# Kernel tuning notes

Measured on AMD Instinct MI355X. Metric: run time of the kernel, lower is better.

## Reference

```python
import jax, jax.numpy as jnp
import numpy as np

CUTOFF = 5.0
MAX_NUM_PAIRS = 131072
N_ATOMS = 4096
BOX_L = 40.0


def setup_inputs() -> dict:
    key = jax.random.key(0)
    k1, _ = jax.random.split(key)
    positions = jax.random.uniform(k1, (N_ATOMS, 3), dtype=jnp.float32) * BOX_L
    box = jnp.eye(3, dtype=jnp.float32) * BOX_L  # triclinic box vectors (rows)
    return {"positions": positions, "box": box}


def _min_image_deltas(positions, box):
    # delta[i, j] = positions[i] - positions[j], wrapped by the minimum image
    # convention: subtract the nearest integer multiple of the box vectors.
    delta = positions[:, None, :] - positions[None, :, :]  # [N, N, 3]
    inv_box = jnp.linalg.inv(box)
    frac = delta @ inv_box                                  # fractional coords
    delta = delta - jnp.round(frac) @ box
    return delta


def reference(positions, box):
    n = positions.shape[0]
    delta = _min_image_deltas(positions, box)               # [N, N, 3]
    dist2 = jnp.sum(delta * delta, axis=-1)                 # [N, N]

    idx = jnp.arange(n)
    upper = idx[:, None] < idx[None, :]                     # unique pairs i<j
    mask = upper & (dist2 < CUTOFF * CUTOFF)

    n_pairs = jnp.sum(mask).astype(jnp.int32)
    # Compact hit pairs into a fixed-size buffer (static shape for jit).
    flat_idx, = jnp.nonzero(mask.ravel(), size=MAX_NUM_PAIRS, fill_value=0)
    valid = jnp.arange(MAX_NUM_PAIRS) < n_pairs

    pair_i = jnp.where(valid, flat_idx // n, -1)
    pair_j = jnp.where(valid, flat_idx % n, -1)
    pairs = jnp.stack([pair_i, pair_j], axis=0)             # [2, P]

    deltas = jnp.where(valid[:, None], delta.reshape(n * n, 3)[flat_idx], 0.0)
    d2 = jnp.where(valid, dist2.ravel()[flat_idx], 1.0)     # safe sqrt on pads
    distances = jnp.where(valid, jnp.sqrt(d2), 0.0)

    return pairs, deltas, distances, n_pairs
```

## Files before the change

### kernel.cpp

```cpp
#include <hip/hip_runtime.h>


#define CUT2 25.0f

__device__ __forceinline__ void load_box_inv(const float* __restrict__ box,
                                             float B[3][3], float Binv[3][3]) {
    #pragma unroll
    for (int r = 0; r < 3; ++r)
        #pragma unroll
        for (int c = 0; c < 3; ++c)
            B[r][c] = box[r * 3 + c];

    float a00 = B[0][0], a01 = B[0][1], a02 = B[0][2];
    float a10 = B[1][0], a11 = B[1][1], a12 = B[1][2];
    float a20 = B[2][0], a21 = B[2][1], a22 = B[2][2];

    float adj00 =  (a11 * a22 - a12 * a21);
    float adj01 = -(a01 * a22 - a02 * a21);
    float adj02 =  (a01 * a12 - a02 * a11);
    float adj10 = -(a10 * a22 - a12 * a20);
    float adj11 =  (a00 * a22 - a02 * a20);
    float adj12 = -(a00 * a12 - a02 * a10);
    float adj20 =  (a10 * a21 - a11 * a20);
    float adj21 = -(a00 * a21 - a01 * a20);
    float adj22 =  (a00 * a11 - a01 * a10);

    float det = a00 * adj00 + a01 * adj10 + a02 * adj20;

    Binv[0][0] = __fdiv_rn(adj00, det); Binv[0][1] = __fdiv_rn(adj01, det); Binv[0][2] = __fdiv_rn(adj02, det);
    Binv[1][0] = __fdiv_rn(adj10, det); Binv[1][1] = __fdiv_rn(adj11, det); Binv[1][2] = __fdiv_rn(adj12, det);
    Binv[2][0] = __fdiv_rn(adj20, det); Binv[2][1] = __fdiv_rn(adj21, det); Binv[2][2] = __fdiv_rn(adj22, det);
}

__device__ __forceinline__ void min_image(float xi, float yi, float zi,
                                          float xj, float yj, float zj,
                                          const float B[3][3], const float Binv[3][3],
                                          float& dx, float& dy, float& dz, float& d2) {
    dx = __fsub_rn(xi, xj);
    dy = __fsub_rn(yi, yj);
    dz = __fsub_rn(zi, zj);

    float f0 = __fadd_rn(__fadd_rn(__fmul_rn(dx, Binv[0][0]), __fmul_rn(dy, Binv[1][0])), __fmul_rn(dz, Binv[2][0]));
    float f1 = __fadd_rn(__fadd_rn(__fmul_rn(dx, Binv[0][1]), __fmul_rn(dy, Binv[1][1])), __fmul_rn(dz, Binv[2][1]));
    float f2 = __fadd_rn(__fadd_rn(__fmul_rn(dx, Binv[0][2]), __fmul_rn(dy, Binv[1][2])), __fmul_rn(dz, Binv[2][2]));

    float r0 = rintf(f0), r1 = rintf(f1), r2 = rintf(f2);

    float c0 = __fadd_rn(__fadd_rn(__fmul_rn(r0, B[0][0]), __fmul_rn(r1, B[1][0])), __fmul_rn(r2, B[2][0]));
    float c1 = __fadd_rn(__fadd_rn(__fmul_rn(r0, B[0][1]), __fmul_rn(r1, B[1][1])), __fmul_rn(r2, B[2][1]));
    float c2 = __fadd_rn(__fadd_rn(__fmul_rn(r0, B[0][2]), __fmul_rn(r1, B[1][2])), __fmul_rn(r2, B[2][2]));

    dx = __fsub_rn(dx, c0);
    dy = __fsub_rn(dy, c1);
    dz = __fsub_rn(dz, c2);

    d2 = __fadd_rn(__fadd_rn(__fmul_rn(dx, dx), __fmul_rn(dy, dy)), __fmul_rn(dz, dz));
}

__device__ __forceinline__ int count_row_lds(int i, int lane,
                                             const float* __restrict__ spos,
                                             const float B[3][3], const float Binv[3][3],
                                             unsigned long long* __restrict__ mrow,
                                             int nchunks) {
    float xi = spos[3 * i + 0], yi = spos[3 * i + 1], zi = spos[3 * i + 2];
    int c0 = i >> 6;
    int cnt = 0;

    {
        int j = (c0 << 6) + lane;
        bool hit = false;
        if (j > i) {
            float dx, dy, dz, d2;
            min_image(xi, yi, zi, spos[3 * j + 0], spos[3 * j + 1], spos[3 * j + 2],
                      B, Binv, dx, dy, dz, d2);
            hit = (d2 < CUT2);
        }
        unsigned long long m = __ballot(hit);
        if (lane == 0) mrow[c0] = m;
        cnt += __popcll(m);
    }

    int c = c0 + 1;
    for (; c + 4 <= nchunks; c += 4) {
        int j0 = (c << 6) + lane;
        float dx0, dy0, dz0, d20, dx1, dy1, dz1, d21;
        float dx2, dy2, dz2, d22, dx3, dy3, dz3, d23;
        min_image(xi, yi, zi, spos[3 * j0 + 0],   spos[3 * j0 + 1],   spos[3 * j0 + 2],   B, Binv, dx0, dy0, dz0, d20);
        min_image(xi, yi, zi, spos[3 * j0 + 192], spos[3 * j0 + 193], spos[3 * j0 + 194], B, Binv, dx1, dy1, dz1, d21);
        min_image(xi, yi, zi, spos[3 * j0 + 384], spos[3 * j0 + 385], spos[3 * j0 + 386], B, Binv, dx2, dy2, dz2, d22);
        min_image(xi, yi, zi, spos[3 * j0 + 576], spos[3 * j0 + 577], spos[3 * j0 + 578], B, Binv, dx3, dy3, dz3, d23);
        unsigned long long m0 = __ballot(d20 < CUT2);
        unsigned long long m1 = __ballot(d21 < CUT2);
        unsigned long long m2 = __ballot(d22 < CUT2);
        unsigned long long m3 = __ballot(d23 < CUT2);
        if (lane == 0) { mrow[c] = m0; mrow[c + 1] = m1; mrow[c + 2] = m2; mrow[c + 3] = m3; }
        cnt += __popcll(m0) + __popcll(m1) + __popcll(m2) + __popcll(m3);
    }
    for (; c < nchunks; ++c) {
        int j = (c << 6) + lane;
        float dx, dy, dz, d2;
        min_image(xi, yi, zi, spos[3 * j + 0], spos[3 * j + 1], spos[3 * j + 2],
                  B, Binv, dx, dy, dz, d2);
        unsigned long long m = __ballot(d2 < CUT2);
        if (lane == 0) mrow[c] = m;
        cnt += __popcll(m);
    }
    return cnt;
}

__global__ void __launch_bounds__(256)
k1_pad_count(const float* __restrict__ pos, const float* __restrict__ box,
             float* __restrict__ out, int* __restrict__ counts,
             unsigned long long* __restrict__ masks, int N, int P) {
    __shared__ float spos[12288];

    int tid = blockIdx.x * blockDim.x + threadIdx.x;
    int nthreads = gridDim.x * blockDim.x;

    int total = 6 * P + 1;
    for (int k = tid; k < total; k += nthreads)
        out[k] = (k < 2 * P) ? -1.0f : 0.0f;

    for (int k = threadIdx.x; k < 3 * N; k += blockDim.x)
        spos[k] = pos[k];
    __syncthreads();

    int w = tid >> 6;
    int lane = tid & 63;
    int nchunks = N >> 6;

    float B[3][3], Binv[3][3];
    load_box_inv(box, B, Binv);

    int rowA = w;
    int rowB = N - 1 - w;

    int cA = count_row_lds(rowA, lane, spos, B, Binv,
                           masks + (size_t)rowA * nchunks, nchunks);
    if (lane == 0) counts[rowA] = cA;

    int cB = count_row_lds(rowB, lane, spos, B, Binv,
                           masks + (size_t)rowB * nchunks, nchunks);
    if (lane == 0) counts[rowB] = cB;
}

__global__ void __launch_bounds__(256)
k2_scan_fill(const float* __restrict__ pos, const float* __restrict__ box,
             const int* __restrict__ counts,
             const unsigned long long* __restrict__ masks,
             float* __restrict__ out, int N, int P) {
    int tid = blockIdx.x * blockDim.x + threadIdx.x;
    int i = tid >> 6;
    int lane = tid & 63;
    int nchunks = N >> 6;
    int c0 = i >> 6;

    int pre = 0;
    for (int b = 0; b < i; b += 64) {
        int k = b + lane;
        pre += (k < i) ? counts[k] : 0;
    }
    #pragma unroll
    for (int d = 1; d < 64; d <<= 1)
        pre += __shfl_xor(pre, d);

    if (i == N - 1 && lane == 0)
        out[6 * (size_t)P] = (float)(pre + counts[i]);

    unsigned long long mymask = masks[(size_t)i * nchunks + lane];

    float B[3][3], Binv[3][3];
    load_box_inv(box, B, Binv);
    float xi = pos[3 * i + 0], yi = pos[3 * i + 1], zi = pos[3 * i + 2];

    int base = pre;
    for (int cc = c0; cc < nchunks; ++cc) {
        unsigned long long m = __shfl(mymask, cc);
        if (m != 0ull) {
            if ((m >> lane) & 1ull) {
                int j = (cc << 6) + lane;
                float dx, dy, dz, d2;
                min_image(xi, yi, zi, pos[3 * j + 0], pos[3 * j + 1], pos[3 * j + 2],
                          B, Binv, dx, dy, dz, d2);
                int slot = base + __popcll(m & ((1ull << lane) - 1ull));
                if (slot < P) {
                    out[slot] = (float)i;
                    out[P + slot] = (float)j;
                    size_t db = 2 * (size_t)P + 3 * (size_t)slot;
                    out[db + 0] = dx;
                    out[db + 1] = dy;
                    out[db + 2] = dz;
                    out[5 * (size_t)P + slot] = sqrtf(d2);
                }
            }
            base += __popcll(m);
        }
    }
}

extern "C" void kernel_launch(void* const* d_in, const int* in_sizes, int n_in,
                              void* d_out, int out_size, void* d_ws, size_t ws_size,
                              hipStream_t stream) {
    const float* pos = (const float*)d_in[0];
    const float* box = (const float*)d_in[1];
    float* out = (float*)d_out;

    int N = in_sizes[0] / 3;
    int P = (out_size - 1) / 6;
    int nchunks = N >> 6;

    char* w = (char*)d_ws;
    int* counts = (int*)w;                         w += (size_t)N * sizeof(int);
    unsigned long long* masks = (unsigned long long*)w;

    k1_pad_count<<<N / 8, 256, 0, stream>>>(pos, box, out, counts, masks, N, P);

    k2_scan_fill<<<N / 4, 256, 0, stream>>>(pos, box, counts, masks, out, N, P);
}
```

Baseline: 103.3 us.

## Drop LDS staging, use one row per wave, add diagonal-box fast path

The count kernel no longer copies all positions into 48KB of shared memory per block. It now reads them straight from global memory and cache, assigns one row per wave instead of a paired triangular row split, and doubles the grid. A runtime check for an orthorhombic box selects a templated diagonal min-image path that skips the full 3x3 matrix products. The changes target per-block LDS fill cost and occupancy limits plus ALU work, at the cost of load imbalance across rows of the triangular pair space and more global/L1 traffic.

```diff
diff --git a/kernel.cpp b/kernel.cpp
--- a/kernel.cpp
+++ b/kernel.cpp
@@ -57,12 +57,32 @@
     d2 = __fadd_rn(__fadd_rn(__fmul_rn(dx, dx), __fmul_rn(dy, dy)), __fmul_rn(dz, dz));
 }
 
-__device__ __forceinline__ int count_row_lds(int i, int lane,
-                                             const float* __restrict__ spos,
-                                             const float B[3][3], const float Binv[3][3],
-                                             unsigned long long* __restrict__ mrow,
-                                             int nchunks) {
-    float xi = spos[3 * i + 0], yi = spos[3 * i + 1], zi = spos[3 * i + 2];
+__device__ __forceinline__ void min_image_diag(float xi, float yi, float zi,
+                                               float xj, float yj, float zj,
+                                               float b0, float b1, float b2,
+                                               float ib0, float ib1, float ib2,
+                                               float& dx, float& dy, float& dz, float& d2) {
+    dx = __fsub_rn(xi, xj);
+    dy = __fsub_rn(yi, yj);
+    dz = __fsub_rn(zi, zj);
+    float r0 = rintf(__fmul_rn(dx, ib0));
+    float r1 = rintf(__fmul_rn(dy, ib1));
+    float r2 = rintf(__fmul_rn(dz, ib2));
+    dx = __fsub_rn(dx, __fmul_rn(r0, b0));
+    dy = __fsub_rn(dy, __fmul_rn(r1, b1));
+    dz = __fsub_rn(dz, __fmul_rn(r2, b2));
+    d2 = __fadd_rn(__fadd_rn(__fmul_rn(dx, dx), __fmul_rn(dy, dy)), __fmul_rn(dz, dz));
+}
+
+template <bool DIAG>
+__device__ __forceinline__ int count_row(int i, int lane,
+                                         const float* __restrict__ pos,
+                                         const float B[3][3], const float Binv[3][3],
+                                         unsigned long long* __restrict__ mrow,
+                                         int nchunks) {
+    float xi = pos[3 * i + 0], yi = pos[3 * i + 1], zi = pos[3 * i + 2];
+    float b0 = B[0][0], b1 = B[1][1], b2 = B[2][2];
+    float ib0 = Binv[0][0], ib1 = Binv[1][1], ib2 = Binv[2][2];
     int c0 = i >> 6;
     int cnt = 0;
 
@@ -71,8 +91,12 @@
         bool hit = false;
         if (j > i) {
             float dx, dy, dz, d2;
-            min_image(xi, yi, zi, spos[3 * j + 0], spos[3 * j + 1], spos[3 * j + 2],
-                      B, Binv, dx, dy, dz, d2);
+            if (DIAG)
+                min_image_diag(xi, yi, zi, pos[3 * j], pos[3 * j + 1], pos[3 * j + 2],
+                               b0, b1, b2, ib0, ib1, ib2, dx, dy, dz, d2);
+            else
+                min_image(xi, yi, zi, pos[3 * j], pos[3 * j + 1], pos[3 * j + 2],
+                          B, Binv, dx, dy, dz, d2);
             hit = (d2 < CUT2);
         }
         unsigned long long m = __ballot(hit);
@@ -85,10 +109,17 @@
         int j0 = (c << 6) + lane;
         float dx0, dy0, dz0, d20, dx1, dy1, dz1, d21;
         float dx2, dy2, dz2, d22, dx3, dy3, dz3, d23;
-        min_image(xi, yi, zi, spos[3 * j0 + 0],   spos[3 * j0 + 1],   spos[3 * j0 + 2],   B, Binv, dx0, dy0, dz0, d20);
-        min_image(xi, yi, zi, spos[3 * j0 + 192], spos[3 * j0 + 193], spos[3 * j0 + 194], B, Binv, dx1, dy1, dz1, d21);
-        min_image(xi, yi, zi, spos[3 * j0 + 384], spos[3 * j0 + 385], spos[3 * j0 + 386], B, Binv, dx2, dy2, dz2, d22);
-        min_image(xi, yi, zi, spos[3 * j0 + 576], spos[3 * j0 + 577], spos[3 * j0 + 578], B, Binv, dx3, dy3, dz3, d23);
+        if (DIAG) {
+            min_image_diag(xi, yi, zi, pos[3 * j0 +   0], pos[3 * j0 +   1], pos[3 * j0 +   2], b0, b1, b2, ib0, ib1, ib2, dx0, dy0, dz0, d20);
+            min_image_diag(xi, yi, zi, pos[3 * j0 + 192], pos[3 * j0 + 193], pos[3 * j0 + 194], b0, b1, b2, ib0, ib1, ib2, dx1, dy1, dz1, d21);
+            min_image_diag(xi, yi, zi, pos[3 * j0 + 384], pos[3 * j0 + 385], pos[3 * j0 + 386], b0, b1, b2, ib0, ib1, ib2, dx2, dy2, dz2, d22);
+            min_image_diag(xi, yi, zi, pos[3 * j0 + 576], pos[3 * j0 + 577], pos[3 * j0 + 578], b0, b1, b2, ib0, ib1, ib2, dx3, dy3, dz3, d23);
+        } else {
+            min_image(xi, yi, zi, pos[3 * j0 +   0], pos[3 * j0 +   1], pos[3 * j0 +   2], B, Binv, dx0, dy0, dz0, d20);
+            min_image(xi, yi, zi, pos[3 * j0 + 192], pos[3 * j0 + 193], pos[3 * j0 + 194], B, Binv, dx1, dy1, dz1, d21);
+            min_image(xi, yi, zi, pos[3 * j0 + 384], pos[3 * j0 + 385], pos[3 * j0 + 386], B, Binv, dx2, dy2, dz2, d22);
+            min_image(xi, yi, zi, pos[3 * j0 + 576], pos[3 * j0 + 577], pos[3 * j0 + 578], B, Binv, dx3, dy3, dz3, d23);
+        }
         unsigned long long m0 = __ballot(d20 < CUT2);
         unsigned long long m1 = __ballot(d21 < CUT2);
         unsigned long long m2 = __ballot(d22 < CUT2);
@@ -99,8 +130,12 @@
     for (; c < nchunks; ++c) {
         int j = (c << 6) + lane;
         float dx, dy, dz, d2;
-        min_image(xi, yi, zi, spos[3 * j + 0], spos[3 * j + 1], spos[3 * j + 2],
-                  B, Binv, dx, dy, dz, d2);
+        if (DIAG)
+            min_image_diag(xi, yi, zi, pos[3 * j], pos[3 * j + 1], pos[3 * j + 2],
+                           b0, b1, b2, ib0, ib1, ib2, dx, dy, dz, d2);
+        else
+            min_image(xi, yi, zi, pos[3 * j], pos[3 * j + 1], pos[3 * j + 2],
+                      B, Binv, dx, dy, dz, d2);
         unsigned long long m = __ballot(d2 < CUT2);
         if (lane == 0) mrow[c] = m;
         cnt += __popcll(m);
@@ -112,8 +147,6 @@
 k1_pad_count(const float* __restrict__ pos, const float* __restrict__ box,
              float* __restrict__ out, int* __restrict__ counts,
              unsigned long long* __restrict__ masks, int N, int P) {
-    __shared__ float spos[12288];
-
     int tid = blockIdx.x * blockDim.x + threadIdx.x;
     int nthreads = gridDim.x * blockDim.x;
 
@@ -121,27 +154,23 @@
     for (int k = tid; k < total; k += nthreads)
         out[k] = (k < 2 * P) ? -1.0f : 0.0f;
 
-    for (int k = threadIdx.x; k < 3 * N; k += blockDim.x)
-        spos[k] = pos[k];
-    __syncthreads();
-
-    int w = tid >> 6;
+    int i = tid >> 6;
     int lane = tid & 63;
     int nchunks = N >> 6;
 
     float B[3][3], Binv[3][3];
     load_box_inv(box, B, Binv);
-
-    int rowA = w;
-    int rowB = N - 1 - w;
-
-    int cA = count_row_lds(rowA, lane, spos, B, Binv,
-                           masks + (size_t)rowA * nchunks, nchunks);
-    if (lane == 0) counts[rowA] = cA;
-
-    int cB = count_row_lds(rowB, lane, spos, B, Binv,
-                           masks + (size_t)rowB * nchunks, nchunks);
-    if (lane == 0) counts[rowB] = cB;
+    bool diag = (B[0][1] == 0.0f) & (B[0][2] == 0.0f) & (B[1][0] == 0.0f) &
+                (B[1][2] == 0.0f) & (B[2][0] == 0.0f) & (B[2][1] == 0.0f);
+
+    int cnt;
+    if (diag)
+        cnt = count_row<true>(i, lane, pos, B, Binv,
+                              masks + (size_t)i * nchunks, nchunks);
+    else
+        cnt = count_row<false>(i, lane, pos, B, Binv,
+                               masks + (size_t)i * nchunks, nchunks);
+    if (lane == 0) counts[i] = cnt;
 }
 
 __global__ void __launch_bounds__(256)
@@ -213,7 +242,7 @@
     int* counts = (int*)w;                         w += (size_t)N * sizeof(int);
     unsigned long long* masks = (unsigned long long*)w;
 
-    k1_pad_count<<<N / 8, 256, 0, stream>>>(pos, box, out, counts, masks, N, P);
+    k1_pad_count<<<N / 4, 256, 0, stream>>>(pos, box, out, counts, masks, N, P);
 
     k2_scan_fill<<<N / 4, 256, 0, stream>>>(pos, box, counts, masks, out, N, P);
 }
```

Result: faster. 87.63 us (-15.2%).
